# Optimization experiments

Measured on AMD Instinct MI355X. Metric: run time of the kernel, lower is better.

The kernel has to match this reference:

```python
import jax, jax.numpy as jnp
import numpy as np

N = 256    # num_neurons
I = 784    # input_dim
H = 128    # hidden_dim
B = 256    # batch
E = 4096   # num edges (sparse topology, fan_out 16)


def setup_inputs() -> dict:
    key = jax.random.key(0)
    k0, k1, k2, k3, k4 = jax.random.split(key, 5)
    x = jax.random.normal(k0, (B, I), dtype=jnp.float32)
    # per-neuron linear weights/biases (AutonomicNeuron modeled as Linear(input_dim, hidden_dim))
    W = jax.random.normal(k1, (N, I, H), dtype=jnp.float32) * (1.0 / np.sqrt(I))
    b = jax.random.normal(k2, (N, H), dtype=jnp.float32) * 0.01
    edge_index = jax.random.randint(k3, (2, E), 0, N)  # (2, E) [src; tgt]
    edge_weights = jax.random.normal(k4, (E,), dtype=jnp.float32) * 0.01  # init scale in _init_*_topology
    return {"x": x, "W": W, "b": b, "edge_index": edge_index, "edge_weights": edge_weights}


def reference(x, W, b, edge_index, edge_weights):
    # per-neuron projection: h0[n] = x @ W[n] + b[n]  -> (N, B, H)
    h0 = jnp.einsum('bi,nih->nbh', x, W) + b[:, None, :]
    src = edge_index[0]
    tgt = edge_index[1]
    # sequential, order-dependent message passing (faithful to the Python edge loop):
    # h[tgt] <- h[tgt] + h[src] * w, using the CURRENT h[src]
    def step(h, sw):
        s, t, w = sw
        h = h.at[t].add(h[s] * w)
        return h, None
    h_final, _ = jax.lax.scan(step, h0, (src, tgt, edge_weights))
    # aggregate: mean over all neurons' hidden states -> (B, H)
    return h_final.mean(axis=0)
```

## Files before the change

kernel.cpp:

```cpp
#include <hip/hip_runtime.h>

#define EDGES 4096
#define NNODES 256

typedef unsigned short u16;

__global__ __launch_bounds__(256) void k1_coeff(const int* __restrict__ ei,
                                                const float* __restrict__ ew,
                                                float* __restrict__ c_out) {
    __shared__ __align__(16) char smem[59648];
    float* w_q    = (float*)(smem);
    u16*   s_e    = (u16*)  (smem + 16384);
    u16*   t_e    = (u16*)  (smem + 24576);
    float* rho    = (float*)(smem + 16384);
    u16*   id_q   = (u16*)  (smem + 32768);
    u16*   t_q    = (u16*)  (smem + 40960);
    float* sfx    = (float*)(smem + 32768);
    u16*   id_u   = (u16*)  (smem + 49152);
    u16*   start_q= (u16*)  (smem + 49152);
    int*   offs   = (int*)  (smem + 57344);
    int*   fillc  = (int*)  (smem + 58372);

    const int tid = threadIdx.x;

    for (int j = tid; j < EDGES; j += 256) {
        s_e[j] = (u16)ei[j];
        t_e[j] = (u16)ei[EDGES + j];
    }
    fillc[tid] = 0;
    __syncthreads();

    for (int j = tid; j < EDGES; j += 256) atomicAdd(&fillc[s_e[j]], 1);
    __syncthreads();

    if (tid < 64) {
        int b0 = tid * 4;
        int c0 = fillc[b0], c1 = fillc[b0 + 1], c2 = fillc[b0 + 2], c3 = fillc[b0 + 3];
        int s  = c0 + c1 + c2 + c3;
        int inc = s;
        #pragma unroll
        for (int d = 1; d < 64; d <<= 1) {
            int v = __shfl_up(inc, d);
            if (tid >= d) inc += v;
        }
        int excl = inc - s;
        offs[b0]     = excl;
        offs[b0 + 1] = excl + c0;
        offs[b0 + 2] = excl + c0 + c1;
        offs[b0 + 3] = excl + c0 + c1 + c2;
        if (tid == 63) offs[256] = inc;
    }
    __syncthreads();

    fillc[tid] = offs[tid];
    __syncthreads();

    for (int j = tid; j < EDGES; j += 256) {
        int pos = atomicAdd(&fillc[s_e[j]], 1);
        id_u[pos] = (u16)j;
    }
    __syncthreads();

    for (int j = tid; j < EDGES; j += 256) {
        int s = s_e[j];
        int lo = offs[s], hi = offs[s + 1];
        int rank = 0;
        for (int q = lo; q < hi; ++q) rank += (id_u[q] < j) ? 1 : 0;
        id_q[lo + rank] = (u16)j;
    }
    __syncthreads();

    for (int q = tid; q < EDGES; q += 256) {
        int e = id_q[q];
        w_q[q] = ew[e];
        t_q[q] = t_e[e];
    }
    __syncthreads();

    for (int q = tid; q < EDGES; q += 256) {
        int myid = id_q[q];
        int t = t_q[q];
        int lo = offs[t], hi = offs[t + 1];
        const int hi0 = hi;
        while (lo < hi) {
            int mid = (lo + hi) >> 1;
            if (id_q[mid] > myid) hi = mid; else lo = mid + 1;
        }
        start_q[q] = (lo < hi0) ? (u16)lo : (u16)0xFFFFu;
    }
    __syncthreads();

    for (int q = tid; q < EDGES; q += 256) rho[q] = 1.0f;
    __syncthreads();

    for (int pass = 0; pass < 5; ++pass) {
        for (int q = tid; q < EDGES; q += 256) sfx[q] = w_q[q] * rho[q];
        __syncthreads();
        {
            int lo = offs[tid], hi = offs[tid + 1];
            float run = 0.0f;
            for (int q = hi - 1; q >= lo; --q) { run += sfx[q]; sfx[q] = run; }
        }
        __syncthreads();
        for (int q = tid; q < EDGES; q += 256) {
            int st = start_q[q];
            rho[q] = 1.0f + ((st != 0xFFFF) ? sfx[st] : 0.0f);
        }
        __syncthreads();
    }

    {
        int lo = offs[tid], hi = offs[tid + 1];
        float acc = 0.0f;
        for (int q = lo; q < hi; ++q) acc += w_q[q] * rho[q];
        c_out[tid] = (1.0f + acc) * (1.0f / 256.0f);
    }
}

__global__ __launch_bounds__(256, 4) void k2_wc(const float* __restrict__ W,
                                                const float* __restrict__ bvec,
                                                const float* __restrict__ c,
                                                float* __restrict__ Wc) {
    const int bx = blockIdx.x;
    const int p  = blockIdx.y;
    const int n0 = p * 64;
    __shared__ float cs[64];

    const int tid = threadIdx.x;
    if (tid < 64) cs[tid] = c[n0 + tid];
    __syncthreads();

    if (bx == 98) {
        if (tid < 32) {
            const float4* b4 = (const float4*)bvec;
            float4 acc = make_float4(0.f, 0.f, 0.f, 0.f);
            #pragma unroll 16
            for (int n = 0; n < 64; ++n) {
                float cn = cs[n];
                float4 v = b4[(n0 + n) * 32 + tid];
                acc.x += cn * v.x; acc.y += cn * v.y;
                acc.z += cn * v.z; acc.w += cn * v.w;
            }
            float* dst = Wc + 784 * 128 + tid * 4;
            atomicAdd(dst + 0, acc.x);
            atomicAdd(dst + 1, acc.y);
            atomicAdd(dst + 2, acc.z);
            atomicAdd(dst + 3, acc.w);
        }
        return;
    }

    const int j  = bx * 256 + tid;
    const int i  = j >> 5;
    const int h4 = j & 31;
    const float4* W4 = (const float4*)W + ((size_t)n0 * 784 + i) * 32 + h4;
    float4 acc = make_float4(0.f, 0.f, 0.f, 0.f);
    #pragma unroll 16
    for (int n = 0; n < 64; ++n) {
        float cn = cs[n];
        float4 v = W4[(size_t)n * (784 * 32)];
        acc.x += cn * v.x; acc.y += cn * v.y;
        acc.z += cn * v.z; acc.w += cn * v.w;
    }
    float* dst = Wc + i * 128 + h4 * 4;
    atomicAdd(dst + 0, acc.x);
    atomicAdd(dst + 1, acc.y);
    atomicAdd(dst + 2, acc.z);
    atomicAdd(dst + 3, acc.w);
}

__global__ __launch_bounds__(256) void k3_gemm(const float* __restrict__ x,
                                               const float* __restrict__ Wc,
                                               float* __restrict__ out) {
    const int blk = blockIdx.x;
    __shared__ float xs[4 * 784];
    const int tid = threadIdx.x;

    const float4* x4  = (const float4*)(x + (size_t)blk * 4 * 784);
    float4*       xs4 = (float4*)xs;
    for (int idx = tid; idx < 4 * 196; idx += 256) xs4[idx] = x4[idx];
    __syncthreads();

    const int h    = tid & 127;
    const int half = tid >> 7;
    const float* xr0 = xs + (half * 2) * 784;
    const float* xr1 = xs + (half * 2 + 1) * 784;

    float a0 = 0.f, a1 = 0.f;
    #pragma unroll 8
    for (int i = 0; i < 784; ++i) {
        float wv = Wc[i * 128 + h];
        a0 += xr0[i] * wv;
        a1 += xr1[i] * wv;
    }
    float bch = Wc[784 * 128 + h];
    out[(size_t)(blk * 4 + half * 2) * 128 + h]     = a0 + bch;
    out[(size_t)(blk * 4 + half * 2 + 1) * 128 + h] = a1 + bch;
}

extern "C" void kernel_launch(void* const* d_in, const int* in_sizes, int n_in,
                              void* d_out, int out_size, void* d_ws, size_t ws_size,
                              hipStream_t stream) {
    const float* x  = (const float*)d_in[0];
    const float* W  = (const float*)d_in[1];
    const float* bv = (const float*)d_in[2];
    const int*   ei = (const int*)d_in[3];
    const float* ew = (const float*)d_in[4];
    float* out = (float*)d_out;

    float* c_ws = (float*)d_ws;
    float* Wc   = (float*)d_ws + 256;

    hipMemsetAsync(Wc, 0, (size_t)785 * 128 * sizeof(float), stream);
    k1_coeff<<<1, 256, 0, stream>>>(ei, ew, c_ws);
    k2_wc<<<dim3(99, 4), 256, 0, stream>>>(W, bv, c_ws, Wc);
    k3_gemm<<<64, 256, 0, stream>>>(x, Wc, out);
}
```

Measured before the change: 237.0 us.

## Fold Wc zeroing into coeff kernel and widen k2/k3 grids

Replaces the separate memset with extra blocks in the coefficient kernel that zero the Wc buffer, saving a launch. The W-reduction kernel splits neurons into 8 groups of 32 instead of 4 of 64 to put more blocks on the GPU, at the cost of more atomics. The final GEMM uses 128 blocks with 2 rows each and four independent accumulators to increase parallelism and ILP, but each Wc load is now reused by only one row.

New measurement: 225.6 us. 4.8% less time.

```diff
diff --git a/kernel.cpp b/kernel.cpp
--- a/kernel.cpp
+++ b/kernel.cpp
@@ -7,7 +7,17 @@
 
 __global__ __launch_bounds__(256) void k1_coeff(const int* __restrict__ ei,
                                                 const float* __restrict__ ew,
-                                                float* __restrict__ c_out) {
+                                                float* __restrict__ c_out,
+                                                float* __restrict__ Wc) {
+    if (blockIdx.x != 0) {
+        float4* w4 = (float4*)Wc;
+        int base = (blockIdx.x - 1) * 785;
+        for (int t = threadIdx.x; t < 785; t += 256) {
+            w4[base + t] = make_float4(0.f, 0.f, 0.f, 0.f);
+        }
+        return;
+    }
+
     __shared__ __align__(16) char smem[59648];
     float* w_q    = (float*)(smem);
     u16*   s_e    = (u16*)  (smem + 16384);
@@ -123,19 +133,19 @@
                                                 float* __restrict__ Wc) {
     const int bx = blockIdx.x;
     const int p  = blockIdx.y;
-    const int n0 = p * 64;
-    __shared__ float cs[64];
+    const int n0 = p * 32;
+    __shared__ float cs[32];
 
     const int tid = threadIdx.x;
-    if (tid < 64) cs[tid] = c[n0 + tid];
+    if (tid < 32) cs[tid] = c[n0 + tid];
     __syncthreads();
 
     if (bx == 98) {
         if (tid < 32) {
             const float4* b4 = (const float4*)bvec;
             float4 acc = make_float4(0.f, 0.f, 0.f, 0.f);
-            #pragma unroll 16
-            for (int n = 0; n < 64; ++n) {
+            #pragma unroll 8
+            for (int n = 0; n < 32; ++n) {
                 float cn = cs[n];
                 float4 v = b4[(n0 + n) * 32 + tid];
                 acc.x += cn * v.x; acc.y += cn * v.y;
@@ -155,8 +165,8 @@
     const int h4 = j & 31;
     const float4* W4 = (const float4*)W + ((size_t)n0 * 784 + i) * 32 + h4;
     float4 acc = make_float4(0.f, 0.f, 0.f, 0.f);
-    #pragma unroll 16
-    for (int n = 0; n < 64; ++n) {
+    #pragma unroll 8
+    for (int n = 0; n < 32; ++n) {
         float cn = cs[n];
         float4 v = W4[(size_t)n * (784 * 32)];
         acc.x += cn * v.x; acc.y += cn * v.y;
@@ -173,29 +183,29 @@
                                                const float* __restrict__ Wc,
                                                float* __restrict__ out) {
     const int blk = blockIdx.x;
-    __shared__ float xs[4 * 784];
+    __shared__ float xs[2 * 784];
     const int tid = threadIdx.x;
 
-    const float4* x4  = (const float4*)(x + (size_t)blk * 4 * 784);
+    const float4* x4  = (const float4*)(x + (size_t)blk * 2 * 784);
     float4*       xs4 = (float4*)xs;
-    for (int idx = tid; idx < 4 * 196; idx += 256) xs4[idx] = x4[idx];
-    __syncthreads();
-
-    const int h    = tid & 127;
-    const int half = tid >> 7;
-    const float* xr0 = xs + (half * 2) * 784;
-    const float* xr1 = xs + (half * 2 + 1) * 784;
-
-    float a0 = 0.f, a1 = 0.f;
-    #pragma unroll 8
-    for (int i = 0; i < 784; ++i) {
-        float wv = Wc[i * 128 + h];
-        a0 += xr0[i] * wv;
-        a1 += xr1[i] * wv;
+    for (int idx = tid; idx < 2 * 196; idx += 256) xs4[idx] = x4[idx];
+    __syncthreads();
+
+    const int h = tid & 127;
+    const int r = tid >> 7;
+    const float* xr = xs + r * 784;
+
+    float a0 = 0.f, a1 = 0.f, a2 = 0.f, a3 = 0.f;
+    #pragma unroll 4
+    for (int ii = 0; ii < 196; ++ii) {
+        const int i = ii * 4;
+        a0 += xr[i + 0] * Wc[(i + 0) * 128 + h];
+        a1 += xr[i + 1] * Wc[(i + 1) * 128 + h];
+        a2 += xr[i + 2] * Wc[(i + 2) * 128 + h];
+        a3 += xr[i + 3] * Wc[(i + 3) * 128 + h];
     }
     float bch = Wc[784 * 128 + h];
-    out[(size_t)(blk * 4 + half * 2) * 128 + h]     = a0 + bch;
-    out[(size_t)(blk * 4 + half * 2 + 1) * 128 + h] = a1 + bch;
+    out[(size_t)(blk * 2 + r) * 128 + h] = (a0 + a1) + (a2 + a3) + bch;
 }
 
 extern "C" void kernel_launch(void* const* d_in, const int* in_sizes, int n_in,
@@ -211,8 +221,7 @@
     float* c_ws = (float*)d_ws;
     float* Wc   = (float*)d_ws + 256;
 
-    hipMemsetAsync(Wc, 0, (size_t)785 * 128 * sizeof(float), stream);
-    k1_coeff<<<1, 256, 0, stream>>>(ei, ew, c_ws);
-    k2_wc<<<dim3(99, 4), 256, 0, stream>>>(W, bv, c_ws, Wc);
-    k3_gemm<<<64, 256, 0, stream>>>(x, Wc, out);
-}
+    k1_coeff<<<33, 256, 0, stream>>>(ei, ew, c_ws, Wc);
+    k2_wc<<<dim3(99, 8), 256, 0, stream>>>(W, bv, c_ws, Wc);
+    k3_gemm<<<128, 256, 0, stream>>>(x, Wc, out);
+}
```
